# Kernel optimization log

Hardware: AMD Instinct MI355X
Metric: run time of the kernel (lower is better)

## Reference

```python
import jax, jax.numpy as jnp
import numpy as np

DIM = 180      # channel dim C
HEADS = 6      # num_heads
WS = 8         # window_size
HIDDEN = int(DIM * 4.0)  # mlp hidden = 720
HEAD_DIM = DIM // HEADS  # 30


def layernorm(x, scale, bias, eps=1e-5):
    m = jnp.mean(x, axis=-1, keepdims=True)
    v = jnp.var(x, axis=-1, keepdims=True)
    return (x - m) * jax.lax.rsqrt(v + eps) * scale + bias


def setup_inputs() -> dict:
    key = jax.random.key(0)
    ks = jax.random.split(key, 16)
    B, H, W = 4, 256, 256
    s = 0.02  # weight init scale for numerical sanity
    return {
        "x": jax.random.normal(ks[0], (B, H * W, DIM), jnp.float32),
        "norm1_scale": jnp.ones((DIM,), jnp.float32),
        "norm1_bias": jnp.zeros((DIM,), jnp.float32),
        "qkv_w": jax.random.normal(ks[1], (DIM, 3 * DIM), jnp.float32) * s,  # [in,out] == torch W.T
        "qkv_b": jax.random.normal(ks[2], (3 * DIM,), jnp.float32) * s,
        "proj_w": jax.random.normal(ks[3], (DIM, DIM), jnp.float32) * s,
        "proj_b": jax.random.normal(ks[4], (DIM,), jnp.float32) * s,
        "norm2_scale": jnp.ones((DIM,), jnp.float32),
        "norm2_bias": jnp.zeros((DIM,), jnp.float32),
        "mlp_w1": jax.random.normal(ks[5], (DIM, HIDDEN), jnp.float32) * s,
        "mlp_b1": jax.random.normal(ks[6], (HIDDEN,), jnp.float32) * s,
        "mlp_w2": jax.random.normal(ks[7], (HIDDEN, DIM), jnp.float32) * s,
        "mlp_b2": jax.random.normal(ks[8], (DIM,), jnp.float32) * s,
        "H": H,
        "W": W,
    }


def reference(x, norm1_scale, norm1_bias, qkv_w, qkv_b, proj_w, proj_b,
              norm2_scale, norm2_bias, mlp_w1, mlp_b1, mlp_w2, mlp_b2, H, W):
    B, L, C = x.shape
    shortcut = x
    h = layernorm(x, norm1_scale, norm1_bias).reshape(B, H, W, C)
    # pad to multiples of window size (no-op when H,W % WS == 0)
    pad_b = (WS - H % WS) % WS
    pad_r = (WS - W % WS) % WS
    h = jnp.pad(h, ((0, 0), (0, pad_b), (0, pad_r), (0, 0)))
    Hp, Wp = H + pad_b, W + pad_r
    # window_partition: (B,Hp,Wp,C) -> (nW*B, WS*WS, C)
    win = h.reshape(B, Hp // WS, WS, Wp // WS, WS, C)
    win = win.transpose(0, 1, 3, 2, 4, 5).reshape(-1, WS * WS, C)
    Bw, N, _ = win.shape
    # fused qkv projection
    qkv = (win @ qkv_w + qkv_b).reshape(Bw, N, 3, HEADS, HEAD_DIM)
    qkv = qkv.transpose(2, 0, 3, 1, 4)  # (3, Bw, heads, N, head_dim)
    q, k, v = qkv[0], qkv[1], qkv[2]
    q = q * (HEAD_DIM ** -0.5)
    attn = jax.nn.softmax(jnp.einsum('bhnd,bhmd->bhnm', q, k), axis=-1)
    o = jnp.einsum('bhnm,bhmd->bhnd', attn, v)
    o = o.transpose(0, 2, 1, 3).reshape(Bw, N, C)
    o = o @ proj_w + proj_b
    # window_reverse: (nW*B, WS*WS, C) -> (B,Hp,Wp,C)
    h = o.reshape(B, Hp // WS, Wp // WS, WS, WS, C)
    h = h.transpose(0, 1, 3, 2, 4, 5).reshape(B, Hp, Wp, C)
    h = h[:, :H, :W, :].reshape(B, H * W, C)
    x = shortcut + h
    # MLP with exact (erf) GELU, matching torch nn.GELU default
    y = layernorm(x, norm2_scale, norm2_bias)
    y = jax.nn.gelu(y @ mlp_w1 + mlp_b1, approximate=False) @ mlp_w2 + mlp_b2
    return x + y
```

## Files before the change

### kernel.cpp

```cpp
#include <hip/hip_runtime.h>

typedef unsigned int u32;
typedef unsigned short u16;
typedef __attribute__((ext_vector_type(8))) __bf16 bf16x8;
typedef __attribute__((ext_vector_type(4))) float f32x4;

#define MFMA(a,b,c) __builtin_amdgcn_mfma_f32_16x16x32_bf16(a,b,c,0,0,0)

__device__ __forceinline__ float bf2f(u16 v){ return __uint_as_float(((u32)v) << 16); }
__device__ __forceinline__ u16 f2bf(float f){
  u32 u = __float_as_uint(f);
  u += 0x7fffu + ((u >> 16) & 1u);
  return (u16)(u >> 16);
}
__device__ __forceinline__ u32 pack2(float a, float b){
  return (u32)f2bf(a) | ((u32)f2bf(b) << 16);
}
__device__ __forceinline__ float gelu_fast(float v){
  float t = v*(-1.5957691216f - 0.0713548163f*v*v);
  return v / (1.f + __expf(t));
}

#define OQKV 0
#define OWP  122880
#define OW1  159744
#define OW2  307200
#define NW_TOT 448512

__global__ void swin_unpack(const float* __restrict__ qkvw, const float* __restrict__ projw,
                            const float* __restrict__ w1, const float* __restrict__ w2,
                            u16* __restrict__ ws){
  int idx = blockIdx.x * 256 + threadIdx.x;
  if (idx >= NW_TOT) return;
  float val = 0.f;
  if (idx < OWP){
    int t = idx, nt = t / 3072, r = t % 3072, kt = r >> 9, e = r & 511;
    int lane = e >> 3, j = e & 7;
    int n = nt*16 + (lane & 15), k = kt*32 + (lane >> 4)*8 + j;
    if (n < 576){
      int p = n / 192, c = n - p*192;
      if (c < 180 && k < 180) val = qkvw[k*540 + p*180 + c];
    }
  } else if (idx < OW1){
    int t = idx - OWP, nt = t / 3072, r = t % 3072, kt = r >> 9, e = r & 511;
    int lane = e >> 3, j = e & 7;
    int n = nt*16 + (lane & 15), k = kt*32 + (lane >> 4)*8 + j;
    if (n < 180 && k < 180) val = projw[k*180 + n];
  } else if (idx < OW2){
    int t = idx - OW1, nt = t / 3072, r = t % 3072, kt = r >> 9, e = r & 511;
    int lane = e >> 3, j = e & 7;
    int n = nt*16 + (lane & 15), k = kt*32 + (lane >> 4)*8 + j;
    if (n < 720 && k < 180) val = w1[k*720 + n];
  } else {
    int t = idx - OW2, nt = t / 11776, r = t % 11776, kt = r >> 9, e = r & 511;
    int lane = e >> 3, j = e & 7;
    int n = nt*16 + (lane & 15), k = kt*32 + (lane >> 4)*8 + j;
    if (n < 180 && k < 720) val = w2[k*180 + n];
  }
  ws[idx] = f2bf(val);
}

#define A_Y   0
#define A_Q   25600
#define A_K   51200
#define A_VT  76800
#define A_P   104448
#define A_RB  132096

__global__ __launch_bounds__(768, 1) void swin_attn(
    const float* __restrict__ x, const float* __restrict__ n1s, const float* __restrict__ n1b,
    const u16* __restrict__ ws, const float* __restrict__ qkvb,
    const float* __restrict__ projb, float* __restrict__ out){
  __shared__ __align__(16) char sm[132352];
  const int tid = threadIdx.x;
  const int w12 = tid >> 6, l = tid & 63, l15 = l & 15, lq = l >> 4;
  int* rb = (int*)(sm + A_RB);
  const f32x4 fz = {0.f, 0.f, 0.f, 0.f};

  if (tid < 64){
    int wb = blockIdx.x;
    int b = wb >> 10, wy = (wb >> 5) & 31, wx = wb & 31;
    rb[tid] = b*65536 + (wy*8 + (tid>>3))*256 + (wx*8 + (tid&7));
  }
  for (int i = tid; i < 2304; i += 768){
    int row = i / 36, t = i - row*36;
    if (t < 24){
      int buf = (t >= 12) ? A_K : A_Q; int tt = t % 12;
      *(u16*)(sm + buf + row*400 + ((tt>>1)*32 + 30 + (tt&1))*2) = 0;
    } else
      *(u16*)(sm + A_Y + row*400 + (180 + t - 24)*2) = 0;
  }
  __syncthreads();

  if (w12 < 8){
    int r3 = l & 7, lq2 = l >> 3;
    int n = w12*8 + r3;
    const float4* px = (const float4*)(x + (size_t)rb[n]*180);
    float4 v[6];
    #pragma unroll
    for (int i = 0; i < 5; ++i) v[i] = px[lq2 + 8*i];
    v[5] = (lq2 < 5) ? px[lq2 + 40] : make_float4(0.f,0.f,0.f,0.f);
    float s = 0.f, ss = 0.f;
    #pragma unroll
    for (int i = 0; i < 6; ++i){
      s  += v[i].x + v[i].y + v[i].z + v[i].w;
      ss += v[i].x*v[i].x + v[i].y*v[i].y + v[i].z*v[i].z + v[i].w*v[i].w;
    }
    #pragma unroll
    for (int m = 8; m <= 32; m <<= 1){ s += __shfl_xor(s, m); ss += __shfl_xor(ss, m); }
    float mean = s * (1.f/180.f);
    float rstd = rsqrtf(ss * (1.f/180.f) - mean*mean + 1e-5f);
    u32* yr = (u32*)(sm + A_Y + n*400);
    const float4* s4 = (const float4*)n1s;
    const float4* b4 = (const float4*)n1b;
    #pragma unroll
    for (int i = 0; i < 6; ++i){
      if (i < 5 || lq2 < 5){
        int c4 = lq2 + 8*i;
        float4 sc = s4[c4], bi = b4[c4];
        float e0 = (v[i].x - mean)*rstd*sc.x + bi.x;
        float e1 = (v[i].y - mean)*rstd*sc.y + bi.y;
        float e2 = (v[i].z - mean)*rstd*sc.z + bi.z;
        float e3 = (v[i].w - mean)*rstd*sc.w + bi.w;
        yr[c4*2]     = pack2(e0, e1);
        yr[c4*2 + 1] = pack2(e2, e3);
      }
    }
  }
  __syncthreads();

  {
    const int ntb = w12*3;
    f32x4 acc[4][3];
    #pragma unroll
    for (int m = 0; m < 4; ++m)
      #pragma unroll
      for (int i = 0; i < 3; ++i) acc[m][i] = fz;
    bf16x8 bcur[3];
    #pragma unroll
    for (int i = 0; i < 3; ++i)
      bcur[i] = *(const bf16x8*)(ws + OQKV + ((ntb+i)*6 + 0)*512 + l*8);
    #pragma unroll
    for (int kt = 0; kt < 6; ++kt){
      bf16x8 bnxt[3];
      if (kt < 5){
        #pragma unroll
        for (int i = 0; i < 3; ++i)
          bnxt[i] = *(const bf16x8*)(ws + OQKV + ((ntb+i)*6 + kt + 1)*512 + l*8);
      }
      bf16x8 a[4];
      #pragma unroll
      for (int m = 0; m < 4; ++m)
        a[m] = *(const bf16x8*)(sm + A_Y + (m*16 + l15)*400 + kt*64 + lq*16);
      #pragma unroll
      for (int m = 0; m < 4; ++m)
        #pragma unroll
        for (int i = 0; i < 3; ++i)
          acc[m][i] = MFMA(a[m], bcur[i], acc[m][i]);
      if (kt < 5){
        #pragma unroll
        for (int i = 0; i < 3; ++i) bcur[i] = bnxt[i];
      }
    }
    #pragma unroll
    for (int i = 0; i < 3; ++i){
      int n = (ntb + i)*16 + l15;
      int p = n / 192, c = n - p*192;
      if (c < 180){
        float bias = qkvb[p*180 + c];
        int h = c / 30, d = c - h*30;
        int colp = h*32 + d;
        #pragma unroll
        for (int m = 0; m < 4; ++m)
          #pragma unroll
          for (int r = 0; r < 4; ++r){
            float val = acc[m][i][r] + bias;
            int tok = m*16 + lq*4 + r;
            if (p == 0)      *(u16*)(sm + A_Q + tok*400 + colp*2) = f2bf(val * 0.18257418583505536f);
            else if (p == 1) *(u16*)(sm + A_K + tok*400 + colp*2) = f2bf(val);
            else             *(u16*)(sm + A_VT + colp*144 + tok*2) = f2bf(val);
          }
      }
    }
  }
  __syncthreads();

  {
    const int tq = w12 & 3, hbase = (w12 >> 2)*2;
    for (int h = hbase; h < hbase + 2; ++h){
      bf16x8 aq = *(const bf16x8*)(sm + A_Q + (tq*16 + l15)*400 + h*64 + lq*16);
      f32x4 s[4];
      #pragma unroll
      for (int nt = 0; nt < 4; ++nt){
        bf16x8 bk = *(const bf16x8*)(sm + A_K + (nt*16 + l15)*400 + h*64 + lq*16);
        s[nt] = MFMA(aq, bk, fz);
      }
      #pragma unroll
      for (int r = 0; r < 4; ++r){
        float mx = fmaxf(fmaxf(s[0][r], s[1][r]), fmaxf(s[2][r], s[3][r]));
        mx = fmaxf(mx, __shfl_xor(mx, 1));
        mx = fmaxf(mx, __shfl_xor(mx, 2));
        mx = fmaxf(mx, __shfl_xor(mx, 4));
        mx = fmaxf(mx, __shfl_xor(mx, 8));
        float e0 = __expf(s[0][r]-mx), e1 = __expf(s[1][r]-mx);
        float e2 = __expf(s[2][r]-mx), e3 = __expf(s[3][r]-mx);
        float sum = e0 + e1 + e2 + e3;
        sum += __shfl_xor(sum,1); sum += __shfl_xor(sum,2);
        sum += __shfl_xor(sum,4); sum += __shfl_xor(sum,8);
        float iv = 1.f / sum;
        char* pr = sm + A_P + w12*2304 + (lq*4 + r)*144 + l15*2;
        *(u16*)(pr)      = f2bf(e0 * iv);
        *(u16*)(pr + 32) = f2bf(e1 * iv);
        *(u16*)(pr + 64) = f2bf(e2 * iv);
        *(u16*)(pr + 96) = f2bf(e3 * iv);
      }
      asm volatile("s_waitcnt lgkmcnt(0)" ::: "memory");
      f32x4 o0 = fz, o1 = fz;
      #pragma unroll
      for (int kt = 0; kt < 2; ++kt){
        bf16x8 aP  = *(const bf16x8*)(sm + A_P + w12*2304 + l15*144 + kt*64 + lq*16);
        bf16x8 bv0 = *(const bf16x8*)(sm + A_VT + (h*32 + l15)*144 + kt*64 + lq*16);
        bf16x8 bv1 = *(const bf16x8*)(sm + A_VT + (h*32 + 16 + l15)*144 + kt*64 + lq*16);
        o0 = MFMA(aP, bv0, o0);
        o1 = MFMA(aP, bv1, o1);
      }
      #pragma unroll
      for (int r = 0; r < 4; ++r){
        int tok = tq*16 + lq*4 + r;
        {
          int col = h*30 + l15;
          *(u16*)(sm + A_Y + tok*400 + col*2) = f2bf(o0[r]);
        }
        if (l15 < 14){
          int col = h*30 + 16 + l15;
          *(u16*)(sm + A_Y + tok*400 + col*2) = f2bf(o1[r]);
        }
      }
    }
  }
  __syncthreads();

  {
    const int mh2 = w12 / 6, ng6 = w12 % 6;
    f32x4 acc[2][2];
    #pragma unroll
    for (int m = 0; m < 2; ++m)
      #pragma unroll
      for (int i = 0; i < 2; ++i) acc[m][i] = fz;
    bf16x8 bcur[2];
    #pragma unroll
    for (int i = 0; i < 2; ++i)
      bcur[i] = *(const bf16x8*)(ws + OWP + ((ng6*2+i)*6 + 0)*512 + l*8);
    #pragma unroll
    for (int kt = 0; kt < 6; ++kt){
      bf16x8 bnxt[2];
      if (kt < 5){
        #pragma unroll
        for (int i = 0; i < 2; ++i)
          bnxt[i] = *(const bf16x8*)(ws + OWP + ((ng6*2+i)*6 + kt + 1)*512 + l*8);
      }
      bf16x8 ah[2];
      #pragma unroll
      for (int m = 0; m < 2; ++m)
        ah[m] = *(const bf16x8*)(sm + A_Y + (mh2*32 + m*16 + l15)*400 + kt*64 + lq*16);
      #pragma unroll
      for (int m = 0; m < 2; ++m)
        #pragma unroll
        for (int i = 0; i < 2; ++i)
          acc[m][i] = MFMA(ah[m], bcur[i], acc[m][i]);
      if (kt < 5){
        #pragma unroll
        for (int i = 0; i < 2; ++i) bcur[i] = bnxt[i];
      }
    }
    float* res = (float*)(sm + A_Q);
    #pragma unroll
    for (int i = 0; i < 2; ++i){
      int col = (ng6*2 + i)*16 + l15;
      if (col < 180){
        float bias = projb[col];
        #pragma unroll
        for (int m = 0; m < 2; ++m)
          #pragma unroll
          for (int r = 0; r < 4; ++r)
            res[(mh2*32 + m*16 + lq*4 + r)*180 + col] = acc[m][i][r] + bias;
      }
    }
  }
  __syncthreads();

  {
    const float4* res4 = (const float4*)(sm + A_Q);
    for (int idx = tid; idx < 2880; idx += 768){
      int n = idx / 45, c4 = idx - n*45;
      size_t g4 = (size_t)rb[n]*45 + c4;
      float4 rv = res4[idx];
      float4 xv = ((const float4*)x)[g4];
      float4 o; o.x = rv.x + xv.x; o.y = rv.y + xv.y; o.z = rv.z + xv.z; o.w = rv.w + xv.w;
      ((float4*)out)[g4] = o;
    }
  }
}

#define M_Y 0
#define M_G 25600

__global__ __launch_bounds__(512, 1) void swin_mlp(
    const float* __restrict__ n2s, const float* __restrict__ n2b,
    const u16* __restrict__ ws, const float* __restrict__ b1, const float* __restrict__ b2,
    float* __restrict__ out){
  __shared__ __align__(16) char sm[124928];
  const int tid = threadIdx.x;
  const int w8 = tid >> 6, l = tid & 63, l15 = l & 15, lq = l >> 4;
  const size_t base = (size_t)blockIdx.x * (64*180);
  const f32x4 fz = {0.f, 0.f, 0.f, 0.f};

  for (int i = tid; i < 768; i += 512){
    int row = i / 12, col = 180 + i % 12;
    *(u16*)(sm + M_Y + row*400 + col*2) = 0;
  }
  {
    int r3 = l & 7, lq2 = l >> 3;
    int n = w8*8 + r3;
    const float4* px = (const float4*)(out + base + (size_t)n*180);
    float4 v[6];
    #pragma unroll
    for (int i = 0; i < 5; ++i) v[i] = px[lq2 + 8*i];
    v[5] = (lq2 < 5) ? px[lq2 + 40] : make_float4(0.f,0.f,0.f,0.f);
    float s = 0.f, ss = 0.f;
    #pragma unroll
    for (int i = 0; i < 6; ++i){
      s  += v[i].x + v[i].y + v[i].z + v[i].w;
      ss += v[i].x*v[i].x + v[i].y*v[i].y + v[i].z*v[i].z + v[i].w*v[i].w;
    }
    #pragma unroll
    for (int m = 8; m <= 32; m <<= 1){ s += __shfl_xor(s, m); ss += __shfl_xor(ss, m); }
    float mean = s * (1.f/180.f);
    float rstd = rsqrtf(ss * (1.f/180.f) - mean*mean + 1e-5f);
    u32* yr = (u32*)(sm + M_Y + n*400);
    const float4* s4 = (const float4*)n2s;
    const float4* b4 = (const float4*)n2b;
    #pragma unroll
    for (int i = 0; i < 6; ++i){
      if (i < 5 || lq2 < 5){
        int c4 = lq2 + 8*i;
        float4 sc = s4[c4], bi = b4[c4];
        float e0 = (v[i].x - mean)*rstd*sc.x + bi.x;
        float e1 = (v[i].y - mean)*rstd*sc.y + bi.y;
        float e2 = (v[i].z - mean)*rstd*sc.z + bi.z;
        float e3 = (v[i].w - mean)*rstd*sc.w + bi.w;
        yr[c4*2]     = pack2(e0, e1);
        yr[c4*2 + 1] = pack2(e2, e3);
      }
    }
  }
  __syncthreads();

  for (int ch = 0; ch < 2; ++ch){
    const int ntb = w8*6 + ch*3;
    f32x4 acc[4][3];
    #pragma unroll
    for (int m = 0; m < 4; ++m)
      #pragma unroll
      for (int i = 0; i < 3; ++i) acc[m][i] = fz;
    bf16x8 wb0[3], wb1[3];
    #pragma unroll
    for (int i = 0; i < 3; ++i){
      wb0[i] = *(const bf16x8*)(ws + OW1 + ((ntb+i)*6 + 0)*512 + l*8);
      wb1[i] = *(const bf16x8*)(ws + OW1 + ((ntb+i)*6 + 1)*512 + l*8);
    }
    #pragma unroll
    for (int kt = 0; kt < 6; ++kt){
      bf16x8 wbn[3];
      if (kt + 2 < 6){
        #pragma unroll
        for (int i = 0; i < 3; ++i)
          wbn[i] = *(const bf16x8*)(ws + OW1 + ((ntb+i)*6 + kt + 2)*512 + l*8);
      }
      bf16x8 a[4];
      #pragma unroll
      for (int m = 0; m < 4; ++m)
        a[m] = *(const bf16x8*)(sm + M_Y + (m*16 + l15)*400 + kt*64 + lq*16);
      #pragma unroll
      for (int m = 0; m < 4; ++m)
        #pragma unroll
        for (int i = 0; i < 3; ++i)
          acc[m][i] = MFMA(a[m], wb0[i], acc[m][i]);
      #pragma unroll
      for (int i = 0; i < 3; ++i){ wb0[i] = wb1[i]; if (kt + 2 < 6) wb1[i] = wbn[i]; }
    }
    #pragma unroll
    for (int i = 0; i < 3; ++i){
      int gc = (ntb + i)*16 + l15;
      float bias = (gc < 720) ? b1[gc] : 0.f;
      #pragma unroll
      for (int m = 0; m < 4; ++m)
        #pragma unroll
        for (int r = 0; r < 4; ++r){
          float v = acc[m][i][r] + bias;
          float gel = (gc < 720) ? gelu_fast(v) : 0.f;
          *(u16*)(sm + M_G + (m*16 + lq*4 + r)*1552 + gc*2) = f2bf(gel);
        }
    }
  }
  __syncthreads();

  {
    const int mh2 = w8 >> 2, wc4 = w8 & 3;
    f32x4 acc2[2][3];
    #pragma unroll
    for (int m = 0; m < 2; ++m)
      #pragma unroll
      for (int i = 0; i < 3; ++i) acc2[m][i] = fz;
    bf16x8 wb0[3], wb1[3];
    #pragma unroll
    for (int i = 0; i < 3; ++i){
      wb0[i] = *(const bf16x8*)(ws + OW2 + ((wc4*3+i)*23 + 0)*512 + l*8);
      wb1[i] = *(const bf16x8*)(ws + OW2 + ((wc4*3+i)*23 + 1)*512 + l*8);
    }
    for (int kt = 0; kt < 23; ++kt){
      bf16x8 wbn[3];
      int ktn = (kt < 21) ? kt + 2 : 22;
      #pragma unroll
      for (int i = 0; i < 3; ++i)
        wbn[i] = *(const bf16x8*)(ws + OW2 + ((wc4*3+i)*23 + ktn)*512 + l*8);
      bf16x8 a[2];
      #pragma unroll
      for (int m = 0; m < 2; ++m)
        a[m] = *(const bf16x8*)(sm + M_G + (mh2*32 + m*16 + l15)*1552 + kt*64 + lq*16);
      #pragma unroll
      for (int m = 0; m < 2; ++m)
        #pragma unroll
        for (int i = 0; i < 3; ++i)
          acc2[m][i] = MFMA(a[m], wb0[i], acc2[m][i]);
      #pragma unroll
      for (int i = 0; i < 3; ++i){ wb0[i] = wb1[i]; wb1[i] = wbn[i]; }
    }
    __syncthreads();

    float* res = (float*)(sm + M_G);
    #pragma unroll
    for (int i = 0; i < 3; ++i){
      int col = (wc4*3 + i)*16 + l15;
      if (col < 180){
        float bias = b2[col];
        #pragma unroll
        for (int m = 0; m < 2; ++m)
          #pragma unroll
          for (int r = 0; r < 4; ++r)
            res[(mh2*32 + m*16 + lq*4 + r)*180 + col] = acc2[m][i][r] + bias;
      }
    }
  }
  __syncthreads();

  {
    const float4* res4 = (const float4*)(sm + M_G);
    float4* og = (float4*)(out + base);
    for (int idx = tid; idx < 2880; idx += 512){
      float4 rv = res4[idx];
      float4 xv = og[idx];
      float4 o; o.x = rv.x + xv.x; o.y = rv.y + xv.y; o.z = rv.z + xv.z; o.w = rv.w + xv.w;
      og[idx] = o;
    }
  }
}

extern "C" void kernel_launch(void* const* d_in, const int* in_sizes, int n_in,
                              void* d_out, int out_size, void* d_ws, size_t ws_size,
                              hipStream_t stream){
  const float* x     = (const float*)d_in[0];
  const float* n1s   = (const float*)d_in[1];
  const float* n1b   = (const float*)d_in[2];
  const float* qkvw  = (const float*)d_in[3];
  const float* qkvb  = (const float*)d_in[4];
  const float* projw = (const float*)d_in[5];
  const float* projb = (const float*)d_in[6];
  const float* n2s   = (const float*)d_in[7];
  const float* n2b   = (const float*)d_in[8];
  const float* w1    = (const float*)d_in[9];
  const float* b1    = (const float*)d_in[10];
  const float* w2    = (const float*)d_in[11];
  const float* b2    = (const float*)d_in[12];
  float* outp = (float*)d_out;
  u16* wsp = (u16*)d_ws;

  swin_unpack<<<(NW_TOT + 255) / 256, 256, 0, stream>>>(qkvw, projw, w1, w2, wsp);
  swin_attn<<<4096, 768, 0, stream>>>(x, n1s, n1b, wsp, qkvb, projb, outp);
  swin_mlp<<<4096, 512, 0, stream>>>(n2s, n2b, wsp, b1, b2, outp);
}
```

Before: 644.7 us.

## Double MLP kernel block to 1024 threads and repartition GEMM work per wave

The MLP kernel now runs 16 waves per block instead of 8. The work is repartitioned: layernorm uses 4 rows per wave, the first GEMM handles 3 column tiles per wave in one pass instead of two chunks, and the second GEMM gives each wave one 16-row tile. Weight prefetch depth in the first GEMM drops from two stages to one, and the GELU division becomes a hardware reciprocal. The aim is more latency hiding within a block, which holds only one block per CU because of its large shared memory. The cost is more register pressure under the 1024-thread bound, and each wave reuses fewer A/B fragments.

```diff
diff --git a/kernel.cpp b/kernel.cpp
--- a/kernel.cpp
+++ b/kernel.cpp
@@ -18,7 +18,7 @@
 }
 __device__ __forceinline__ float gelu_fast(float v){
   float t = v*(-1.5957691216f - 0.0713548163f*v*v);
-  return v / (1.f + __expf(t));
+  return v * __builtin_amdgcn_rcpf(1.f + __expf(t));
 }
 
 #define OQKV 0
@@ -305,45 +305,45 @@
 #define M_Y 0
 #define M_G 25600
 
-__global__ __launch_bounds__(512, 1) void swin_mlp(
+__global__ __launch_bounds__(1024, 1) void swin_mlp(
     const float* __restrict__ n2s, const float* __restrict__ n2b,
     const u16* __restrict__ ws, const float* __restrict__ b1, const float* __restrict__ b2,
     float* __restrict__ out){
   __shared__ __align__(16) char sm[124928];
   const int tid = threadIdx.x;
-  const int w8 = tid >> 6, l = tid & 63, l15 = l & 15, lq = l >> 4;
+  const int w16 = tid >> 6, l = tid & 63, l15 = l & 15, lq = l >> 4;
   const size_t base = (size_t)blockIdx.x * (64*180);
   const f32x4 fz = {0.f, 0.f, 0.f, 0.f};
 
-  for (int i = tid; i < 768; i += 512){
-    int row = i / 12, col = 180 + i % 12;
+  if (tid < 768){
+    int row = tid / 12, col = 180 + tid % 12;
     *(u16*)(sm + M_Y + row*400 + col*2) = 0;
   }
   {
-    int r3 = l & 7, lq2 = l >> 3;
-    int n = w8*8 + r3;
+    int r4 = l & 3, lq4 = l >> 2;
+    int n = w16*4 + r4;
     const float4* px = (const float4*)(out + base + (size_t)n*180);
-    float4 v[6];
-    #pragma unroll
-    for (int i = 0; i < 5; ++i) v[i] = px[lq2 + 8*i];
-    v[5] = (lq2 < 5) ? px[lq2 + 40] : make_float4(0.f,0.f,0.f,0.f);
+    float4 v[3];
+    v[0] = px[lq4];
+    v[1] = px[lq4 + 16];
+    v[2] = (lq4 < 13) ? px[lq4 + 32] : make_float4(0.f,0.f,0.f,0.f);
     float s = 0.f, ss = 0.f;
     #pragma unroll
-    for (int i = 0; i < 6; ++i){
+    for (int i = 0; i < 3; ++i){
       s  += v[i].x + v[i].y + v[i].z + v[i].w;
       ss += v[i].x*v[i].x + v[i].y*v[i].y + v[i].z*v[i].z + v[i].w*v[i].w;
     }
     #pragma unroll
-    for (int m = 8; m <= 32; m <<= 1){ s += __shfl_xor(s, m); ss += __shfl_xor(ss, m); }
+    for (int m = 4; m <= 32; m <<= 1){ s += __shfl_xor(s, m); ss += __shfl_xor(ss, m); }
     float mean = s * (1.f/180.f);
     float rstd = rsqrtf(ss * (1.f/180.f) - mean*mean + 1e-5f);
     u32* yr = (u32*)(sm + M_Y + n*400);
     const float4* s4 = (const float4*)n2s;
     const float4* b4 = (const float4*)n2b;
     #pragma unroll
-    for (int i = 0; i < 6; ++i){
-      if (i < 5 || lq2 < 5){
-        int c4 = lq2 + 8*i;
+    for (int i = 0; i < 3; ++i){
+      if (i < 2 || lq4 < 13){
+        int c4 = lq4 + 16*i;
         float4 sc = s4[c4], bi = b4[c4];
         float e0 = (v[i].x - mean)*rstd*sc.x + bi.x;
         float e1 = (v[i].y - mean)*rstd*sc.y + bi.y;
@@ -356,26 +356,24 @@
   }
   __syncthreads();
 
-  for (int ch = 0; ch < 2; ++ch){
-    const int ntb = w8*6 + ch*3;
+  {
+    const int ntb = w16*3;
     f32x4 acc[4][3];
     #pragma unroll
     for (int m = 0; m < 4; ++m)
       #pragma unroll
       for (int i = 0; i < 3; ++i) acc[m][i] = fz;
-    bf16x8 wb0[3], wb1[3];
-    #pragma unroll
-    for (int i = 0; i < 3; ++i){
-      wb0[i] = *(const bf16x8*)(ws + OW1 + ((ntb+i)*6 + 0)*512 + l*8);
-      wb1[i] = *(const bf16x8*)(ws + OW1 + ((ntb+i)*6 + 1)*512 + l*8);
-    }
+    bf16x8 bcur[3];
+    #pragma unroll
+    for (int i = 0; i < 3; ++i)
+      bcur[i] = *(const bf16x8*)(ws + OW1 + ((ntb+i)*6 + 0)*512 + l*8);
     #pragma unroll
     for (int kt = 0; kt < 6; ++kt){
-      bf16x8 wbn[3];
-      if (kt + 2 < 6){
+      bf16x8 bnxt[3];
+      if (kt < 5){
         #pragma unroll
         for (int i = 0; i < 3; ++i)
-          wbn[i] = *(const bf16x8*)(ws + OW1 + ((ntb+i)*6 + kt + 2)*512 + l*8);
+          bnxt[i] = *(const bf16x8*)(ws + OW1 + ((ntb+i)*6 + kt + 1)*512 + l*8);
       }
       bf16x8 a[4];
       #pragma unroll
@@ -385,9 +383,11 @@
       for (int m = 0; m < 4; ++m)
         #pragma unroll
         for (int i = 0; i < 3; ++i)
-          acc[m][i] = MFMA(a[m], wb0[i], acc[m][i]);
-      #pragma unroll
-      for (int i = 0; i < 3; ++i){ wb0[i] = wb1[i]; if (kt + 2 < 6) wb1[i] = wbn[i]; }
+          acc[m][i] = MFMA(a[m], bcur[i], acc[m][i]);
+      if (kt < 5){
+        #pragma unroll
+        for (int i = 0; i < 3; ++i) bcur[i] = bnxt[i];
+      }
     }
     #pragma unroll
     for (int i = 0; i < 3; ++i){
@@ -406,33 +406,26 @@
   __syncthreads();
 
   {
-    const int mh2 = w8 >> 2, wc4 = w8 & 3;
-    f32x4 acc2[2][3];
-    #pragma unroll
-    for (int m = 0; m < 2; ++m)
-      #pragma unroll
-      for (int i = 0; i < 3; ++i) acc2[m][i] = fz;
+    const int mq = w16 & 3, ng = w16 >> 2;
+    f32x4 acc2[3];
+    #pragma unroll
+    for (int i = 0; i < 3; ++i) acc2[i] = fz;
     bf16x8 wb0[3], wb1[3];
     #pragma unroll
     for (int i = 0; i < 3; ++i){
-      wb0[i] = *(const bf16x8*)(ws + OW2 + ((wc4*3+i)*23 + 0)*512 + l*8);
-      wb1[i] = *(const bf16x8*)(ws + OW2 + ((wc4*3+i)*23 + 1)*512 + l*8);
+      wb0[i] = *(const bf16x8*)(ws + OW2 + ((ng*3+i)*23 + 0)*512 + l*8);
+      wb1[i] = *(const bf16x8*)(ws + OW2 + ((ng*3+i)*23 + 1)*512 + l*8);
     }
     for (int kt = 0; kt < 23; ++kt){
       bf16x8 wbn[3];
       int ktn = (kt < 21) ? kt + 2 : 22;
       #pragma unroll
       for (int i = 0; i < 3; ++i)
-        wbn[i] = *(const bf16x8*)(ws + OW2 + ((wc4*3+i)*23 + ktn)*512 + l*8);
-      bf16x8 a[2];
-      #pragma unroll
-      for (int m = 0; m < 2; ++m)
-        a[m] = *(const bf16x8*)(sm + M_G + (mh2*32 + m*16 + l15)*1552 + kt*64 + lq*16);
-      #pragma unroll
-      for (int m = 0; m < 2; ++m)
-        #pragma unroll
-        for (int i = 0; i < 3; ++i)
-          acc2[m][i] = MFMA(a[m], wb0[i], acc2[m][i]);
+        wbn[i] = *(const bf16x8*)(ws + OW2 + ((ng*3+i)*23 + ktn)*512 + l*8);
+      bf16x8 a = *(const bf16x8*)(sm + M_G + (mq*16 + l15)*1552 + kt*64 + lq*16);
+      #pragma unroll
+      for (int i = 0; i < 3; ++i)
+        acc2[i] = MFMA(a, wb0[i], acc2[i]);
       #pragma unroll
       for (int i = 0; i < 3; ++i){ wb0[i] = wb1[i]; wb1[i] = wbn[i]; }
     }
@@ -441,14 +434,12 @@
     float* res = (float*)(sm + M_G);
     #pragma unroll
     for (int i = 0; i < 3; ++i){
-      int col = (wc4*3 + i)*16 + l15;
+      int col = (ng*3 + i)*16 + l15;
       if (col < 180){
         float bias = b2[col];
         #pragma unroll
-        for (int m = 0; m < 2; ++m)
-          #pragma unroll
-          for (int r = 0; r < 4; ++r)
-            res[(mh2*32 + m*16 + lq*4 + r)*180 + col] = acc2[m][i][r] + bias;
+        for (int r = 0; r < 4; ++r)
+          res[(mq*16 + lq*4 + r)*180 + col] = acc2[i][r] + bias;
       }
     }
   }
@@ -457,7 +448,7 @@
   {
     const float4* res4 = (const float4*)(sm + M_G);
     float4* og = (float4*)(out + base);
-    for (int idx = tid; idx < 2880; idx += 512){
+    for (int idx = tid; idx < 2880; idx += 1024){
       float4 rv = res4[idx];
       float4 xv = og[idx];
       float4 o; o.x = rv.x + xv.x; o.y = rv.y + xv.y; o.z = rv.z + xv.z; o.w = rv.w + xv.w;
@@ -487,5 +478,5 @@
 
   swin_unpack<<<(NW_TOT + 255) / 256, 256, 0, stream>>>(qkvw, projw, w1, w2, wsp);
   swin_attn<<<4096, 768, 0, stream>>>(x, n1s, n1b, wsp, qkvb, projb, outp);
-  swin_mlp<<<4096, 512, 0, stream>>>(n2s, n2b, wsp, b1, b2, outp);
-}
+  swin_mlp<<<4096, 1024, 0, stream>>>(n2s, n2b, wsp, b1, b2, outp);
+}
```

Measured after the change: 611.1 us. 1.05x faster.
